# Kernel optimization log

Hardware: AMD Instinct MI355X
Metric: run time of the kernel (lower is better)

## Reference

```python
import jax, jax.numpy as jnp
import numpy as np

N = 50000
E = 1600000
IN_DIM = 128
OUT_DIM = 128
HEADS = 4
C = OUT_DIM // HEADS  # per-head channels = 32
EDGE_DIM = 16
NEG_SLOPE = 0.2
LN_EPS = 1e-5


def setup_inputs() -> dict:
    key = jax.random.key(0)
    ks = jax.random.split(key, 12)
    s = 1.0 / np.sqrt(IN_DIM)
    return {
        "x": jax.random.normal(ks[0], (N, IN_DIM), dtype=jnp.float32),
        "edge_index": jax.random.randint(ks[1], (2, E), 0, N, dtype=jnp.int64),
        "edge_attr": jax.random.normal(ks[2], (E, EDGE_DIM), dtype=jnp.float32),
        # GATv2Conv params
        "W_l": jax.random.normal(ks[3], (IN_DIM, HEADS * C), dtype=jnp.float32) * s,
        "b_l": jnp.zeros((HEADS * C,), dtype=jnp.float32),
        "W_r": jax.random.normal(ks[4], (IN_DIM, HEADS * C), dtype=jnp.float32) * s,
        "b_r": jnp.zeros((HEADS * C,), dtype=jnp.float32),
        "W_e": jax.random.normal(ks[5], (EDGE_DIM, HEADS * C), dtype=jnp.float32) * (1.0 / np.sqrt(EDGE_DIM)),
        "att": jax.random.normal(ks[6], (HEADS, C), dtype=jnp.float32) * (1.0 / np.sqrt(C)),
        "conv_bias": jnp.zeros((HEADS * C,), dtype=jnp.float32),
        # LayerNorm params
        "gamma": jnp.ones((OUT_DIM,), dtype=jnp.float32),
        "beta": jnp.zeros((OUT_DIM,), dtype=jnp.float32),
    }


def _gat_layer(x, edge_index, edge_attr, W_l, b_l, W_r, b_r, W_e, att, conv_bias, gamma, beta):
    src, dst = edge_index[0], edge_index[1]
    # linear projections -> [N, H, C] / [E, H, C]
    x_l = (x @ W_l + b_l).reshape(N, HEADS, C)  # source-side
    x_r = (x @ W_r + b_r).reshape(N, HEADS, C)  # target-side
    e_f = (edge_attr @ W_e).reshape(E, HEADS, C)
    # GATv2 attention logits per edge/head
    z = x_l[src] + x_r[dst] + e_f                      # [E, H, C]
    z = jnp.where(z >= 0, z, NEG_SLOPE * z)            # LeakyReLU(0.2)
    logits = jnp.einsum('ehc,hc->eh', z, att)          # [E, H]
    # segment softmax over incoming edges of each target node
    m = jax.ops.segment_max(logits, dst, num_segments=N)          # [N, H]
    m = jnp.where(jnp.isfinite(m), m, 0.0)
    ex = jnp.exp(logits - m[dst])                                  # [E, H]
    denom = jax.ops.segment_sum(ex, dst, num_segments=N)          # [N, H]
    alpha = ex / (denom[dst] + 1e-16)                              # [E, H]
    # weighted message aggregation (dropout on alpha skipped: eval mode)
    msg = x_l[src] * alpha[:, :, None]                             # [E, H, C]
    out = jax.ops.segment_sum(msg, dst, num_segments=N)           # [N, H, C]
    out = out.reshape(N, HEADS * C) + conv_bias                    # concat heads
    # LayerNorm -> ReLU -> (dropout: identity) -> residual (Identity since in==out)
    mu = jnp.mean(out, axis=-1, keepdims=True)
    var = jnp.mean(jnp.square(out - mu), axis=-1, keepdims=True)
    out = (out - mu) * jax.lax.rsqrt(var + LN_EPS) * gamma + beta
    out = jax.nn.relu(out)
    return out + x


def reference(x, edge_index, edge_attr, W_l, b_l, W_r, b_r, W_e, att, conv_bias, gamma, beta):
    return _gat_layer(x, edge_index, edge_attr, W_l, b_l, W_r, b_r, W_e, att, conv_bias, gamma, beta)
```

## Files before the change

kernel.cpp:

```cpp
#include <hip/hip_runtime.h>
#include <hip/hip_bf16.h>

#define NPB 16
#define EPB 128

__device__ __forceinline__ float b2f(__hip_bfloat16 v) { return __bfloat162float(v); }
__device__ __forceinline__ float ldf(const void* p, long i, int f32) {
    return f32 ? ((const float*)p)[i] : b2f(((const __hip_bfloat16*)p)[i]);
}
__device__ __forceinline__ float bflo(unsigned u) { union { unsigned i; float f; } v; v.i = u << 16; return v.f; }
__device__ __forceinline__ float bfhi(unsigned u) { union { unsigned i; float f; } v; v.i = u & 0xffff0000u; return v.f; }
__device__ __forceinline__ float2 ldf2(const void* p, long i2, int f32) {
    if (f32) return ((const float2*)p)[i2];
    unsigned u = ((const unsigned*)p)[i2];
    return make_float2(bflo(u), bfhi(u));
}
__device__ __forceinline__ int ldi(const int* p, long i, int i32) {
    return i32 ? p[i] : p[2 * i];
}

__global__ void zero_i(int* __restrict__ a, long n, int* __restrict__ dt)
{
    long i = (long)blockIdx.x * 256 + threadIdx.x;
    long stride = (long)gridDim.x * 256;
    for (; i < n; i += stride) a[i] = 0;
    if (blockIdx.x == 0 && threadIdx.x == 0 && dt) { dt[0] = 0; dt[1] = 0; }
}

__global__ void fail_stamp(float* __restrict__ out, float code)
{
    if (threadIdx.x == 0 && blockIdx.x == 0) out[0] = code;
}

__global__ void detect_kernel(const void* __restrict__ x, const int* __restrict__ ei,
                              int* __restrict__ dt, int E_)
{
    int t = threadIdx.x;
    const unsigned short* xb = (const unsigned short*)x;
    int f32 = 0;
    for (int i = t; i < 4096; i += 256) {
        int ex = (xb[i] >> 7) & 0xFF;
        if (ex > 140) f32 = 1;
    }
    if (f32) atomicOr(&dt[0], 1);
    int nz = 0;
    for (int i = t; i < 2048; i += 256) nz |= ei[2 * i + 1];
    if (nz) atomicOr(&dt[1], 1);
}

__global__ __launch_bounds__(128) void gemm_xlr(
    const void* __restrict__ x,
    const void* __restrict__ Wl, const void* __restrict__ bl,
    const void* __restrict__ Wr, const void* __restrict__ br,
    const int* __restrict__ dt,
    __hip_bfloat16* __restrict__ xl, __hip_bfloat16* __restrict__ xr, int n)
{
    __shared__ float xs[NPB][128];
    int f32 = dt[0];
    int t = threadIdx.x;
    int n0 = blockIdx.x * NPB;
    for (int j = 0; j < NPB; ++j) {
        int node = n0 + j;
        xs[j][t] = (node < n) ? ldf(x, (long)node * 128 + t, f32) : 0.f;
    }
    __syncthreads();
    float accl[NPB], accr[NPB];
#pragma unroll
    for (int j = 0; j < NPB; ++j) { accl[j] = 0.f; accr[j] = 0.f; }
    for (int k = 0; k < 128; ++k) {
        float wl = ldf(Wl, k * 128 + t, f32);
        float wr = ldf(Wr, k * 128 + t, f32);
#pragma unroll
        for (int j = 0; j < NPB; ++j) {
            float xv = xs[j][k];
            accl[j] = fmaf(xv, wl, accl[j]);
            accr[j] = fmaf(xv, wr, accr[j]);
        }
    }
    float blv = ldf(bl, t, f32);
    float brv = ldf(br, t, f32);
    for (int j = 0; j < NPB; ++j) {
        int node = n0 + j;
        if (node < n) {
            xl[(long)node * 128 + t] = __float2bfloat16(accl[j] + blv);
            xr[(long)node * 128 + t] = __float2bfloat16(accr[j] + brv);
        }
    }
}

__global__ void hist_kernel(const int* __restrict__ ei, const int* __restrict__ dt,
                            int* __restrict__ cnt, int E_, int N_)
{
    long e = (long)blockIdx.x * 256 + threadIdx.x;
    if (e >= E_) return;
    int d = ldi(ei, E_ + e, dt[1]);
    if ((unsigned)d < (unsigned)N_) atomicAdd(&cnt[d], 1);
}

__global__ __launch_bounds__(1024) void scan_kernel(
    const int* __restrict__ cnt, int* __restrict__ row_ptr, int* __restrict__ fill, int n)
{
    __shared__ int wsum[16];
    __shared__ int carry_s;
    int t = threadIdx.x; int lane = t & 63; int w = t >> 6;
    if (t == 0) { carry_s = 0; row_ptr[0] = 0; }
    __syncthreads();
    for (int base = 0; base < n; base += 1024) {
        int idx = base + t;
        int v = (idx < n) ? cnt[idx] : 0;
        int s = v;
        for (int o = 1; o < 64; o <<= 1) { int u = __shfl_up(s, o, 64); if (lane >= o) s += u; }
        if (lane == 63) wsum[w] = s;
        __syncthreads();
        int carry = carry_s;
        if (w == 0) {
            int ws = (lane < 16) ? wsum[lane] : 0;
            for (int o = 1; o < 16; o <<= 1) { int u = __shfl_up(ws, o, 64); if (lane >= o) ws += u; }
            if (lane < 16) wsum[lane] = ws;
        }
        __syncthreads();
        int woff = (w > 0) ? wsum[w - 1] : 0;
        int incl = s + woff;
        if (idx < n) { row_ptr[idx + 1] = carry + incl; fill[idx] = carry + incl - v; }
        __syncthreads();
        if (t == 0) carry_s = carry + wsum[15];
        __syncthreads();
    }
}

__global__ __launch_bounds__(256) void edge_csr(
    const int* __restrict__ ei, const int* __restrict__ dt,
    const void* __restrict__ ea, const void* __restrict__ We, const void* __restrict__ att,
    const __hip_bfloat16* __restrict__ xl, const __hip_bfloat16* __restrict__ xr,
    int* __restrict__ fill, int* __restrict__ src_sorted, float* __restrict__ lsorted,
    int E_, int N_)
{
    __shared__ float4 ea_s4[EPB][4];
    __shared__ int   src_s[EPB], dst_s[EPB], pos_s[EPB];
    int t = threadIdx.x;
    int f32 = dt[0], i32 = dt[1];
    int w = t >> 6;
    int j = t & 63;
    int h = j >> 4;

    float We0[16], We1[16];
#pragma unroll
    for (int k = 0; k < 16; ++k) {
        float2 v = ldf2(We, (long)k * 64 + j, f32);
        We0[k] = v.x; We1[k] = v.y;
    }
    float2 attv = ldf2(att, j, f32);

    long e0 = (long)blockIdx.x * EPB;
    float* eaf = (float*)ea_s4;
    for (int i = t; i < EPB * 16; i += 256) {
        long e = e0 + (i >> 4);
        eaf[i] = (e < E_) ? ldf(ea, e * 16 + (i & 15), f32) : 0.f;
    }
    if (t < EPB) {
        long e = e0 + t;
        if (e < E_) {
            int s = ldi(ei, e, i32);
            int d = ldi(ei, E_ + e, i32);
            src_s[t] = s; dst_s[t] = d;
            pos_s[t] = ((unsigned)d < (unsigned)N_ && (unsigned)s < (unsigned)N_)
                         ? atomicAdd(&fill[d], 1) : -1;
        } else pos_s[t] = -1;
    }
    __syncthreads();

    const unsigned* xlu = (const unsigned*)xl;
    const unsigned* xru = (const unsigned*)xr;
    for (int it = 0; it < EPB / 4; ++it) {
        int le = (it << 2) | w;
        int pos = pos_s[le];
        if (pos < 0) continue;
        int s = src_s[le], d = dst_s[le];
        unsigned ul = xlu[(long)s * 64 + j];
        unsigned ur = xru[(long)d * 64 + j];
        float z0 = bflo(ul) + bflo(ur);
        float z1 = bfhi(ul) + bfhi(ur);
#pragma unroll
        for (int k = 0; k < 4; ++k) {
            float4 a = ea_s4[le][k];
            z0 = fmaf(a.x, We0[4 * k + 0], z0); z1 = fmaf(a.x, We1[4 * k + 0], z1);
            z0 = fmaf(a.y, We0[4 * k + 1], z0); z1 = fmaf(a.y, We1[4 * k + 1], z1);
            z0 = fmaf(a.z, We0[4 * k + 2], z0); z1 = fmaf(a.z, We1[4 * k + 2], z1);
            z0 = fmaf(a.w, We0[4 * k + 3], z0); z1 = fmaf(a.w, We1[4 * k + 3], z1);
        }
        z0 = (z0 >= 0.f) ? z0 : 0.2f * z0;
        z1 = (z1 >= 0.f) ? z1 : 0.2f * z1;
        float v = fmaf(z1, attv.y, z0 * attv.x);
#pragma unroll
        for (int o = 8; o >= 1; o >>= 1) v += __shfl_xor(v, o, 64);
        if ((j & 15) == 0) lsorted[(long)pos * 4 + h] = __expf(v);
        if (j == 0) src_sorted[pos] = s;
    }
}

__global__ __launch_bounds__(256) void node_csr(
    const int* __restrict__ row_ptr, const int* __restrict__ src_sorted,
    const float* __restrict__ lsorted, const __hip_bfloat16* __restrict__ xl,
    const void* __restrict__ cb, const void* __restrict__ gamma,
    const void* __restrict__ beta, const void* __restrict__ x,
    const int* __restrict__ dt, float* __restrict__ out, int N_)
{
    int w = threadIdx.x >> 6, j = threadIdx.x & 63;
    int n = blockIdx.x * 4 + w;
    if (n >= N_) return;
    int f32 = dt[0];
    int h = j >> 4;
    int beg = row_ptr[n], end = row_ptr[n + 1];
    float acc0 = 0.f, acc1 = 0.f, den = 0.f;
    const unsigned* xlu = (const unsigned*)xl;
    int i = beg;
    for (; i + 1 < end; i += 2) {
        int s0 = src_sorted[i], s1 = src_sorted[i + 1];
        float e0 = lsorted[(long)i * 4 + h];
        float e1 = lsorted[(long)(i + 1) * 4 + h];
        unsigned u0 = xlu[(long)s0 * 64 + j];
        unsigned u1 = xlu[(long)s1 * 64 + j];
        acc0 = fmaf(e0, bflo(u0), acc0); acc1 = fmaf(e0, bfhi(u0), acc1);
        acc0 = fmaf(e1, bflo(u1), acc0); acc1 = fmaf(e1, bfhi(u1), acc1);
        den += e0 + e1;
    }
    if (i < end) {
        int s0 = src_sorted[i];
        float e0 = lsorted[(long)i * 4 + h];
        unsigned u0 = xlu[(long)s0 * 64 + j];
        acc0 = fmaf(e0, bflo(u0), acc0); acc1 = fmaf(e0, bfhi(u0), acc1);
        den += e0;
    }
    float rden = 1.f / (den + 1e-16f);
    float2 cbv = ldf2(cb, j, f32);
    float o0 = acc0 * rden + cbv.x;
    float o1 = acc1 * rden + cbv.y;

    float s = o0 + o1;
#pragma unroll
    for (int o = 1; o < 64; o <<= 1) s += __shfl_xor(s, o, 64);
    float mu = s * (1.f / 128.f);
    float d0 = o0 - mu, d1 = o1 - mu;
    float vs = d0 * d0 + d1 * d1;
#pragma unroll
    for (int o = 1; o < 64; o <<= 1) vs += __shfl_xor(vs, o, 64);
    float rs = rsqrtf(vs * (1.f / 128.f) + 1e-5f);
    float2 gv = ldf2(gamma, j, f32);
    float2 bv = ldf2(beta, j, f32);
    float2 xv = ldf2(x, (long)n * 64 + j, f32);
    float y0 = fmaxf(d0 * rs * gv.x + bv.x, 0.f) + xv.x;
    float y1 = fmaxf(d1 * rs * gv.y + bv.y, 0.f) + xv.y;
    *(float2*)(out + (long)n * 128 + 2 * j) = make_float2(y0, y1);
}

extern "C" void kernel_launch(void* const* d_in, const int* in_sizes, int n_in,
                              void* d_out, int out_size, void* d_ws, size_t ws_size,
                              hipStream_t stream) {
    const void* x     = d_in[0];
    const int*  ei    = (const int*)d_in[1];
    const void* ea    = d_in[2];
    const void* Wl    = d_in[3];
    const void* bl    = d_in[4];
    const void* Wr    = d_in[5];
    const void* br    = d_in[6];
    const void* We    = d_in[7];
    const void* att   = d_in[8];
    const void* cb    = d_in[9];
    const void* gamma = d_in[10];
    const void* beta  = d_in[11];
    float* out = (float*)d_out;

    const int N_ = in_sizes[0] / 128;
    const int E_ = in_sizes[2] / 16;

    size_t need = 0;
    auto sz = [&](size_t b) { size_t r = need; need += (b + 255) & ~(size_t)255; return r; };
    size_t o_xl   = sz((size_t)N_ * 128 * 2);
    size_t o_xr   = sz((size_t)N_ * 128 * 2);
    size_t o_cnt  = sz((size_t)N_ * 4);
    size_t o_row  = sz((size_t)(N_ + 1) * 4);
    size_t o_fill = sz((size_t)N_ * 4);
    size_t o_dt   = sz(256);
    size_t o_src  = sz((size_t)E_ * 4);
    size_t o_lsr  = sz((size_t)E_ * 16);

    if (need > ws_size) {
        fail_stamp<<<1, 64, 0, stream>>>(out, 16384.f);
        return;
    }
    char* p = (char*)d_ws;
    __hip_bfloat16* xl   = (__hip_bfloat16*)(p + o_xl);
    __hip_bfloat16* xr   = (__hip_bfloat16*)(p + o_xr);
    int*   cnt           = (int*)(p + o_cnt);
    int*   row_ptr       = (int*)(p + o_row);
    int*   fill          = (int*)(p + o_fill);
    int*   dt            = (int*)(p + o_dt);
    int*   src_sorted    = (int*)(p + o_src);
    float* lsorted       = (float*)(p + o_lsr);

    zero_i<<<256, 256, 0, stream>>>(cnt, N_, dt);
    detect_kernel<<<1, 256, 0, stream>>>(x, ei, dt, E_);
    gemm_xlr<<<(N_ + NPB - 1) / NPB, 128, 0, stream>>>(x, Wl, bl, Wr, br, dt, xl, xr, N_);
    hist_kernel<<<(E_ + 255) / 256, 256, 0, stream>>>(ei, dt, cnt, E_, N_);
    scan_kernel<<<1, 1024, 0, stream>>>(cnt, row_ptr, fill, N_);
    edge_csr<<<(E_ + EPB - 1) / EPB, 256, 0, stream>>>(ei, dt, ea, We, att, xl, xr,
                                                       fill, src_sorted, lsorted, E_, N_);
    node_csr<<<(N_ + 3) / 4, 256, 0, stream>>>(row_ptr, src_sorted, lsorted, xl,
                                               cb, gamma, beta, x, dt, out, N_);
}
```

Baseline: 768.5 us.

## Load edge attributes per wave directly, use DPP reductions and scalarized gathers

The edge kernel drops the shared-memory staging of edge attributes. Each wave now loads its edge's 16 features straight from global memory with vector loads, and the block size doubles to 256 edges. Edge indices are made wave-uniform with readfirstlane, and the 16-lane shuffle reduction becomes DPP adds. The node kernel unrolls its gather loop to 4 neighbors and scalarizes the source row addresses. Together these aim to cut LDS traffic, barriers and shuffle latency and to raise memory-level parallelism, at the cost of redundant broadcast loads of edge attributes across lanes.

```diff
diff --git a/kernel.cpp b/kernel.cpp
--- a/kernel.cpp
+++ b/kernel.cpp
@@ -2,7 +2,7 @@
 #include <hip/hip_bf16.h>
 
 #define NPB 16
-#define EPB 128
+#define EPB 256
 
 __device__ __forceinline__ float b2f(__hip_bfloat16 v) { return __bfloat162float(v); }
 __device__ __forceinline__ float ldf(const void* p, long i, int f32) {
@@ -17,6 +17,12 @@
 }
 __device__ __forceinline__ int ldi(const int* p, long i, int i32) {
     return i32 ? p[i] : p[2 * i];
+}
+
+template <int CTRL>
+__device__ __forceinline__ float dpp_add(float v) {
+    int s = __builtin_amdgcn_update_dpp(0, __float_as_int(v), CTRL, 0xF, 0xF, true);
+    return v + __int_as_float(s);
 }
 
 __global__ void zero_i(int* __restrict__ a, long n, int* __restrict__ dt)
@@ -135,11 +141,10 @@
     int* __restrict__ fill, int* __restrict__ src_sorted, float* __restrict__ lsorted,
     int E_, int N_)
 {
-    __shared__ float4 ea_s4[EPB][4];
-    __shared__ int   src_s[EPB], dst_s[EPB], pos_s[EPB];
+    __shared__ int src_s[EPB], dst_s[EPB], pos_s[EPB];
     int t = threadIdx.x;
     int f32 = dt[0], i32 = dt[1];
-    int w = t >> 6;
+    int wu = __builtin_amdgcn_readfirstlane(t >> 6);
     int j = t & 63;
     int h = j >> 4;
 
@@ -152,12 +157,7 @@
     float2 attv = ldf2(att, j, f32);
 
     long e0 = (long)blockIdx.x * EPB;
-    float* eaf = (float*)ea_s4;
-    for (int i = t; i < EPB * 16; i += 256) {
-        long e = e0 + (i >> 4);
-        eaf[i] = (e < E_) ? ldf(ea, e * 16 + (i & 15), f32) : 0.f;
-    }
-    if (t < EPB) {
+    {
         long e = e0 + t;
         if (e < E_) {
             int s = ldi(ei, e, i32);
@@ -172,27 +172,44 @@
     const unsigned* xlu = (const unsigned*)xl;
     const unsigned* xru = (const unsigned*)xr;
     for (int it = 0; it < EPB / 4; ++it) {
-        int le = (it << 2) | w;
-        int pos = pos_s[le];
+        int le = (it << 2) | wu;
+        int pos = __builtin_amdgcn_readfirstlane(pos_s[le]);
         if (pos < 0) continue;
-        int s = src_s[le], d = dst_s[le];
-        unsigned ul = xlu[(long)s * 64 + j];
-        unsigned ur = xru[(long)d * 64 + j];
+        int s = __builtin_amdgcn_readfirstlane(src_s[le]);
+        int d = __builtin_amdgcn_readfirstlane(dst_s[le]);
+        unsigned ul = (xlu + ((long)s << 6))[j];
+        unsigned ur = (xru + ((long)d << 6))[j];
+        long e = e0 + le;
+        float a[16];
+        if (f32) {
+            const float4* q = (const float4*)((const float*)ea + e * 16);
+            float4 q0 = q[0], q1 = q[1], q2 = q[2], q3 = q[3];
+            a[0]=q0.x; a[1]=q0.y; a[2]=q0.z; a[3]=q0.w;
+            a[4]=q1.x; a[5]=q1.y; a[6]=q1.z; a[7]=q1.w;
+            a[8]=q2.x; a[9]=q2.y; a[10]=q2.z; a[11]=q2.w;
+            a[12]=q3.x; a[13]=q3.y; a[14]=q3.z; a[15]=q3.w;
+        } else {
+            const uint4* q = (const uint4*)((const __hip_bfloat16*)ea + e * 16);
+            uint4 q0 = q[0], q1 = q[1];
+            a[0]=bflo(q0.x); a[1]=bfhi(q0.x); a[2]=bflo(q0.y); a[3]=bfhi(q0.y);
+            a[4]=bflo(q0.z); a[5]=bfhi(q0.z); a[6]=bflo(q0.w); a[7]=bfhi(q0.w);
+            a[8]=bflo(q1.x); a[9]=bfhi(q1.x); a[10]=bflo(q1.y); a[11]=bfhi(q1.y);
+            a[12]=bflo(q1.z); a[13]=bfhi(q1.z); a[14]=bflo(q1.w); a[15]=bfhi(q1.w);
+        }
         float z0 = bflo(ul) + bflo(ur);
         float z1 = bfhi(ul) + bfhi(ur);
 #pragma unroll
-        for (int k = 0; k < 4; ++k) {
-            float4 a = ea_s4[le][k];
-            z0 = fmaf(a.x, We0[4 * k + 0], z0); z1 = fmaf(a.x, We1[4 * k + 0], z1);
-            z0 = fmaf(a.y, We0[4 * k + 1], z0); z1 = fmaf(a.y, We1[4 * k + 1], z1);
-            z0 = fmaf(a.z, We0[4 * k + 2], z0); z1 = fmaf(a.z, We1[4 * k + 2], z1);
-            z0 = fmaf(a.w, We0[4 * k + 3], z0); z1 = fmaf(a.w, We1[4 * k + 3], z1);
-        }
-        z0 = (z0 >= 0.f) ? z0 : 0.2f * z0;
-        z1 = (z1 >= 0.f) ? z1 : 0.2f * z1;
+        for (int k = 0; k < 16; ++k) {
+            z0 = fmaf(a[k], We0[k], z0);
+            z1 = fmaf(a[k], We1[k], z1);
+        }
+        z0 = fmaxf(z0, 0.2f * z0);
+        z1 = fmaxf(z1, 0.2f * z1);
         float v = fmaf(z1, attv.y, z0 * attv.x);
-#pragma unroll
-        for (int o = 8; o >= 1; o >>= 1) v += __shfl_xor(v, o, 64);
+        v = dpp_add<0xB1>(v);
+        v = dpp_add<0x4E>(v);
+        v = dpp_add<0x124>(v);
+        v = dpp_add<0x128>(v);
         if ((j & 15) == 0) lsorted[(long)pos * 4 + h] = __expf(v);
         if (j == 0) src_sorted[pos] = s;
     }
@@ -214,20 +231,28 @@
     float acc0 = 0.f, acc1 = 0.f, den = 0.f;
     const unsigned* xlu = (const unsigned*)xl;
     int i = beg;
-    for (; i + 1 < end; i += 2) {
-        int s0 = src_sorted[i], s1 = src_sorted[i + 1];
+    for (; i + 3 < end; i += 4) {
+        int s0 = src_sorted[i],     s1 = src_sorted[i + 1];
+        int s2 = src_sorted[i + 2], s3 = src_sorted[i + 3];
         float e0 = lsorted[(long)i * 4 + h];
         float e1 = lsorted[(long)(i + 1) * 4 + h];
-        unsigned u0 = xlu[(long)s0 * 64 + j];
-        unsigned u1 = xlu[(long)s1 * 64 + j];
+        float e2 = lsorted[(long)(i + 2) * 4 + h];
+        float e3 = lsorted[(long)(i + 3) * 4 + h];
+        const unsigned* r0 = xlu + ((long)__builtin_amdgcn_readfirstlane(s0) << 6);
+        const unsigned* r1 = xlu + ((long)__builtin_amdgcn_readfirstlane(s1) << 6);
+        const unsigned* r2 = xlu + ((long)__builtin_amdgcn_readfirstlane(s2) << 6);
+        const unsigned* r3 = xlu + ((long)__builtin_amdgcn_readfirstlane(s3) << 6);
+        unsigned u0 = r0[j], u1 = r1[j], u2 = r2[j], u3 = r3[j];
         acc0 = fmaf(e0, bflo(u0), acc0); acc1 = fmaf(e0, bfhi(u0), acc1);
         acc0 = fmaf(e1, bflo(u1), acc0); acc1 = fmaf(e1, bfhi(u1), acc1);
-        den += e0 + e1;
-    }
-    if (i < end) {
+        acc0 = fmaf(e2, bflo(u2), acc0); acc1 = fmaf(e2, bfhi(u2), acc1);
+        acc0 = fmaf(e3, bflo(u3), acc0); acc1 = fmaf(e3, bfhi(u3), acc1);
+        den += (e0 + e1) + (e2 + e3);
+    }
+    for (; i < end; ++i) {
         int s0 = src_sorted[i];
         float e0 = lsorted[(long)i * 4 + h];
-        unsigned u0 = xlu[(long)s0 * 64 + j];
+        unsigned u0 = (xlu + ((long)__builtin_amdgcn_readfirstlane(s0) << 6))[j];
         acc0 = fmaf(e0, bflo(u0), acc0); acc1 = fmaf(e0, bfhi(u0), acc1);
         den += e0;
     }
```

Result: no change. 757.8 us (-1.4%).
